# Performance work log

Hardware: AMD Instinct MI355X
Metric: run time of the kernel (lower is better)

The kernel has to match this reference:

```python
import jax, jax.numpy as jnp
import numpy as np

B, S, D, H, E, TOP_K = 4, 2048, 1024, 2048, 8, 2


def setup_inputs() -> dict:
    key = jax.random.key(0)
    ks = jax.random.split(key, 5)
    scale_d = 1.0 / np.sqrt(D)
    scale_h = 1.0 / np.sqrt(H)
    return {
        "x": jax.random.normal(ks[0], (B, S, D), dtype=jnp.float32),
        "gate_w": jax.random.normal(ks[1], (D, E), dtype=jnp.float32) * scale_d,
        "w1": jax.random.normal(ks[2], (E, D, H), dtype=jnp.float32) * scale_d,
        "w2": jax.random.normal(ks[3], (E, D, H), dtype=jnp.float32) * scale_d,
        "w3": jax.random.normal(ks[4], (E, H, D), dtype=jnp.float32) * scale_h,
    }


def reference(x, gate_w, w1, w2, w3):
    # Gating: softmax over experts, keep top-k probs, renormalize.
    gate_scores = jax.nn.softmax(x @ gate_w, axis=-1)          # [B,S,E]
    top_vals, top_idx = jax.lax.top_k(gate_scores, TOP_K)      # [B,S,K]
    mask = (jax.nn.one_hot(top_idx, E, dtype=x.dtype) * top_vals[..., None]).sum(axis=-2)  # [B,S,E]
    weights = mask / (mask.sum(axis=-1, keepdims=True) + 1e-9)
    # Dense SwiGLU over ALL experts (faithful to the original ModuleList loop).
    g = jax.nn.silu(jnp.einsum('bsd,edh->bseh', x, w1)) * jnp.einsum('bsd,edh->bseh', x, w2)  # [B,S,E,H]
    expert_out = jnp.einsum('bseh,ehd->bsed', g, w3)           # [B,S,E,D]
    # Masked weighted combine (dropout is identity in eval / p=0).
    return jnp.einsum('bse,bsed->bsd', weights, expert_out)    # [B,S,D]
```

## Files before the change

### kernel.cpp

```cpp
#include <hip/hip_runtime.h>

#define T_TOK 8192
#define DDIM 1024
#define HDIM 2048
#define NEXP 8

typedef __attribute__((ext_vector_type(8))) short short8;
typedef __attribute__((ext_vector_type(4))) float f32x4;

#define WAITV2 asm volatile("s_waitcnt vmcnt(2)" ::: "memory")
#define WAITV0 asm volatile("s_waitcnt vmcnt(0)" ::: "memory")
#define WAITL0 asm volatile("s_waitcnt lgkmcnt(0)" ::: "memory")
#define SCHEDB __builtin_amdgcn_sched_barrier(0)
#define BARRIER __builtin_amdgcn_s_barrier()

__device__ __forceinline__ unsigned short f2bf(float f) {
  unsigned int u = __builtin_bit_cast(unsigned int, f);
  u += 0x7fffu + ((u >> 16) & 1u);
  return (unsigned short)(u >> 16);
}
__device__ __forceinline__ float bf2f(unsigned short h) {
  unsigned int u = ((unsigned int)h) << 16;
  return __builtin_bit_cast(float, u);
}
__device__ __forceinline__ void gload16(const void* g, void* l) {
  __builtin_amdgcn_global_load_lds((const __attribute__((address_space(1))) void*)g,
                                   (__attribute__((address_space(3))) void*)l, 16, 0, 0);
}
__device__ __forceinline__ int imin(int a, int b) { return a < b ? a : b; }

__global__ __launch_bounds__(256) void cvt_kernel(const float* __restrict__ in,
                                                  unsigned short* __restrict__ out, int n) {
  int i = (blockIdx.x * 256 + threadIdx.x) * 8;
  int stride = gridDim.x * 256 * 8;
  for (; i < n; i += stride) {
    float4 a = *(const float4*)(in + i);
    float4 b = *(const float4*)(in + i + 4);
    alignas(16) unsigned short t[8] = {f2bf(a.x), f2bf(a.y), f2bf(a.z), f2bf(a.w),
                                       f2bf(b.x), f2bf(b.y), f2bf(b.z), f2bf(b.w)};
    *(uint4*)(out + i) = *(const uint4*)t;
  }
}

__global__ __launch_bounds__(256) void tcvt_kernel(const float* __restrict__ in,
                                                   unsigned short* __restrict__ out,
                                                   int R, int C, size_t outEstride,
                                                   int perm, int s16) {
  int e = blockIdx.z;
  int rb = blockIdx.y * 64, cb = blockIdx.x * 64;
  const float* inE = in + (size_t)e * R * C;
  unsigned short* outE = out + (size_t)e * outEstride;
  __shared__ float tile[64][65];
  int tid = threadIdx.x;
  #pragma unroll
  for (int i = 0; i < 4; ++i) {
    int f = tid + i * 256;
    int r = f >> 4, c4 = (f & 15) << 2;
    float4 v = *(const float4*)(inE + (size_t)(rb + r) * C + cb + c4);
    tile[r][c4] = v.x; tile[r][c4 + 1] = v.y; tile[r][c4 + 2] = v.z; tile[r][c4 + 3] = v.w;
  }
  __syncthreads();
  #pragma unroll
  for (int i = 0; i < 2; ++i) {
    int g = tid + i * 256;
    int oc = g >> 3;
    int r8 = (g & 7) << 3;
    alignas(16) unsigned short tmp[8];
    #pragma unroll
    for (int j = 0; j < 8; ++j) tmp[j] = f2bf(tile[r8 + j][oc]);
    int orow = cb + oc;
    int orow2 = perm ? (32 * (orow >> 4) + (orow & 15) + s16) : orow;
    *(uint4*)(outE + (size_t)orow2 * R + rb + r8) = *(const uint4*)tmp;
  }
}

__global__ __launch_bounds__(256) void gate_kernel(const float* __restrict__ x,
                                                   const float* __restrict__ gw,
                                                   int* __restrict__ t_exp,
                                                   float* __restrict__ t_w) {
  int t = blockIdx.x * 4 + (threadIdx.x >> 6);
  int lane = threadIdx.x & 63;
  const float* xp = x + (size_t)t * DDIM;
  float acc[NEXP];
  #pragma unroll
  for (int e = 0; e < NEXP; ++e) acc[e] = 0.f;
  for (int i = 0; i < DDIM / 64; ++i) {
    int d = i * 64 + lane;
    float xv = xp[d];
    const float* g = gw + d * NEXP;
    #pragma unroll
    for (int e = 0; e < NEXP; ++e) acc[e] += xv * g[e];
  }
  #pragma unroll
  for (int off = 32; off > 0; off >>= 1) {
    #pragma unroll
    for (int e = 0; e < NEXP; ++e) acc[e] += __shfl_xor(acc[e], off, 64);
  }
  float mx = acc[0];
  #pragma unroll
  for (int e = 1; e < NEXP; ++e) mx = fmaxf(mx, acc[e]);
  float p[NEXP]; float S = 0.f;
  #pragma unroll
  for (int e = 0; e < NEXP; ++e) { p[e] = expf(acc[e] - mx); S += p[e]; }
  int i0 = 0; float v0 = p[0];
  #pragma unroll
  for (int e = 1; e < NEXP; ++e) if (p[e] > v0) { v0 = p[e]; i0 = e; }
  int i1 = -1; float v1 = -1.f;
  #pragma unroll
  for (int e = 0; e < NEXP; ++e) if (e != i0 && p[e] > v1) { v1 = p[e]; i1 = e; }
  float pv0 = v0 / S, pv1 = v1 / S;
  float denom = pv0 + pv1 + 1e-9f;
  if (lane == 0) {
    t_exp[t * 2] = i0; t_exp[t * 2 + 1] = i1;
    t_w[t * 2] = pv0 / denom; t_w[t * 2 + 1] = pv1 / denom;
  }
}

__global__ __launch_bounds__(1024) void partition_kernel(
    const int* __restrict__ t_exp, const float* __restrict__ t_w,
    int* __restrict__ ctrl, int* __restrict__ row_tok,
    float* __restrict__ row_w, int* __restrict__ inv_row) {
  int tid = threadIdx.x;
  int wv = tid >> 6, lane = tid & 63;
  __shared__ int wtot[16][8];
  __shared__ int wbase[16][8];
  __shared__ int soff[8];

  int t0 = tid * 8;
  int exps[16];
  int c[8];
  #pragma unroll
  for (int e = 0; e < 8; ++e) c[e] = 0;
  #pragma unroll
  for (int s = 0; s < 16; ++s) {
    exps[s] = t_exp[t0 * 2 + s];
    #pragma unroll
    for (int e = 0; e < 8; ++e) c[e] += (exps[s] == e);
  }
  int inc[8];
  #pragma unroll
  for (int e = 0; e < 8; ++e) inc[e] = c[e];
  #pragma unroll
  for (int d = 1; d < 64; d <<= 1) {
    #pragma unroll
    for (int e = 0; e < 8; ++e) {
      int v = __shfl_up(inc[e], d, 64);
      if (lane >= d) inc[e] += v;
    }
  }
  if (lane == 63) {
    #pragma unroll
    for (int e = 0; e < 8; ++e) wtot[wv][e] = inc[e];
  }
  __syncthreads();
  if (wv == 0 && lane < 16) {
    #pragma unroll
    for (int e = 0; e < 8; ++e) {
      int b = 0;
      for (int w = 0; w < 16; ++w)
        if (w < lane) b += wtot[w][e];
      wbase[lane][e] = b;
    }
  }
  __syncthreads();
  if (tid == 0) {
    int o = 0;
    #pragma unroll
    for (int e = 0; e < 8; ++e) {
      int tot = wbase[15][e] + wtot[15][e];
      ctrl[e] = tot; ctrl[8 + e] = o; soff[e] = o; o += tot;
    }
  }
  __syncthreads();
  int base[8];
  #pragma unroll
  for (int e = 0; e < 8; ++e) base[e] = soff[e] + wbase[wv][e] + (inc[e] - c[e]);
  #pragma unroll
  for (int s = 0; s < 16; ++s) {
    int ee = exps[s];
    float w = t_w[t0 * 2 + s];
    int pos = 0;
    #pragma unroll
    for (int e = 0; e < 8; ++e)
      if (ee == e) { pos = base[e]; base[e] = base[e] + 1; }
    row_tok[pos] = t0 + (s >> 1);
    row_w[pos] = w;
    inv_row[t0 * 2 + s] = pos;
  }
}


#define PHASE(B_, KS_, MH_, STG) do {                                      \
    short8 av[4];                                                          \
    if (MH_ == 0) {                                                        \
      _Pragma("unroll")                                                    \
      for (int n = 0; n < 4; ++n)                                          \
        bv[n] = *(const short8*)(&lds[B_][1][0] + bR + cK[KS_] + n * 1024);\
    }                                                                      \
    _Pragma("unroll")                                                      \
    for (int m = 0; m < 4; ++m)                                            \
      av[m] = *(const short8*)(&lds[B_][0][0] + aR + cK[KS_] + (MH_ * 4 + m) * 1024); \
    STG;                                                                   \
    WAITV2;                                                                \
    BARRIER;                                                               \
    WAITL0; SCHEDB;                                                        \
    __builtin_amdgcn_s_setprio(1);                                         \
    _Pragma("unroll")                                                      \
    for (int m = 0; m < 4; ++m)                                            \
      _Pragma("unroll")                                                    \
      for (int n = 0; n < 4; ++n)                                          \
        acc[MH_ * 4 + m][n] = __builtin_amdgcn_mfma_f32_16x16x32_bf16(av[m], bv[n], acc[MH_ * 4 + m][n], 0, 0, 0); \
    __builtin_amdgcn_s_setprio(0);                                         \
    BARRIER;                                                               \
} while (0)

#define K_PIPELINE(NT)                                                     \
  WAITV0;                                                                  \
  STB(0, 0, 0); STB(0, 1, 0); STB(0, 2, 0); STB(0, 3, 0);                  \
  STA(0, 0, 0); STA(0, 1, 0); STA(0, 2, 0); STA(0, 3, 0);                  \
  WAITV0; BARRIER;                                                         \
  _Pragma("unroll 1")                                                      \
  for (int kt = 0; kt < (NT); kt += 2) {                                   \
    int t1 = kt + 1;                                                       \
    int t2 = imin(kt + 2, (NT) - 1);                                       \
    PHASE(0, 0, 0, { STB(1, 0, t1); STB(1, 1, t1); });                     \
    PHASE(0, 0, 1, { STB(1, 2, t1); STB(1, 3, t1); });                     \
    PHASE(0, 1, 0, { STA(1, 0, t1); STA(1, 2, t1); });                     \
    PHASE(0, 1, 1, { STA(1, 1, t1); STA(1, 3, t1); });                     \
    PHASE(1, 0, 0, { STB(0, 0, t2); STB(0, 1, t2); });                     \
    PHASE(1, 0, 1, { STB(0, 2, t2); STB(0, 3, t2); });                     \
    PHASE(1, 1, 0, { STA(0, 0, t2); STA(0, 2, t2); });                     \
    PHASE(1, 1, 1, { STA(0, 1, t2); STA(0, 3, t2); });                     \
  }

__global__ __launch_bounds__(512, 1) void gemm1_kernel(
    const unsigned short* __restrict__ xbf,
    const unsigned short* __restrict__ w12t,
    const int* __restrict__ row_tok, const float* __restrict__ row_w,
    const int* __restrict__ ctrl, unsigned short* __restrict__ G) {
  int bid = blockIdx.x;
  int e = bid & 7;
  int j = bid >> 3;
  int nt = ((j >> 5) << 2) | (j & 3);
  int mt0 = (j >> 2) & 7;
  int cnt = ctrl[e];
  if (mt0 * 256 >= cnt) return;
  int off = ctrl[8 + e];

  __shared__ unsigned short lds[2][2][16384];

  int tid = threadIdx.x, lane = tid & 63;
  const unsigned short* w12e = w12t + (size_t)e * (4096 * 1024);

  int sr = tid >> 3;
  int cS8 = ((tid & 7) ^ (sr & 7)) * 8;
  const unsigned short* bQ = w12e + (size_t)(nt * 256 + sr) * 1024 + cS8;

  int wid = tid >> 6, wr = wid >> 2, wc = wid & 3;
  int lr16 = lane & 15, hi = lane >> 4;
  int cK[2] = { ((hi) ^ (lr16 & 7)) * 8, ((4 | hi) ^ (lr16 & 7)) * 8 };
  int aR = (wr * 128 + lr16) * 64;
  int bR = (wc * 64 + lr16) * 64;

#define STA(B_, Q_, KT) gload16(aQ[Q_] + (KT) * 64, &lds[B_][0][0] + (Q_) * 4096 + tid * 8)
#define STB(B_, Q_, KT) gload16(bQ + (Q_) * 65536 + (KT) * 64, &lds[B_][1][0] + (Q_) * 4096 + tid * 8)

  #pragma unroll 1
  for (int mt = mt0; mt * 256 < cnt; mt += 8) {
    const unsigned short* aQ[4];
    #pragma unroll
    for (int q = 0; q < 4; ++q) {
      int tok = row_tok[off + imin(mt * 256 + q * 64 + sr, cnt - 1)];
      aQ[q] = xbf + (size_t)tok * 1024 + cS8;
    }
    f32x4 z = {0.f, 0.f, 0.f, 0.f};
    f32x4 acc[8][4];
    #pragma unroll
    for (int m = 0; m < 8; ++m)
      #pragma unroll
      for (int n = 0; n < 4; ++n) acc[m][n] = z;
    short8 bv[4];

    K_PIPELINE(16)

    #pragma unroll
    for (int m = 0; m < 8; ++m)
      #pragma unroll
      for (int jj = 0; jj < 4; ++jj) {
        int rl = mt * 256 + ((m >> 2) ? (64 + wr * 128) : (wr * 128)) + (m & 3) * 16 + hi * 4 + jj;
        rl = mt * 256 + wr * 128 + (m >> 2) * 64 + (m & 3) * 16 + hi * 4 + jj;
        if (rl < cnt) {
          float wrj = row_w[off + rl];
          size_t base = (size_t)(off + rl) * HDIM + nt * 128 + wc * 32 + lr16;
          float h1 = acc[m][0][jj], h2 = acc[m][1][jj];
          G[base] = f2bf((h1 / (1.f + __expf(-h1))) * h2 * wrj);
          h1 = acc[m][2][jj]; h2 = acc[m][3][jj];
          G[base + 16] = f2bf((h1 / (1.f + __expf(-h1))) * h2 * wrj);
        }
      }
  }
#undef STA
#undef STB
}

__global__ __launch_bounds__(512, 1) void gemm2_kernel(
    const unsigned short* __restrict__ G,
    const unsigned short* __restrict__ w3t,
    const int* __restrict__ ctrl, unsigned short* __restrict__ Y) {
  int bid = blockIdx.x;
  int e = bid & 7;
  int j = bid >> 3;
  int nt = j >> 3;
  int mt0 = j & 7;
  int cnt = ctrl[e];
  if (mt0 * 256 >= cnt) return;
  int off = ctrl[8 + e];

  __shared__ unsigned short lds[2][2][16384];

  int tid = threadIdx.x, lane = tid & 63;
  const unsigned short* w3e = w3t + (size_t)e * (1024 * 2048);

  int sr = tid >> 3;
  int cS8 = ((tid & 7) ^ (sr & 7)) * 8;
  const unsigned short* bQ = w3e + (size_t)(nt * 256 + sr) * 2048 + cS8;

  int wid = tid >> 6, wr = wid >> 2, wc = wid & 3;
  int lr16 = lane & 15, hi = lane >> 4;
  int cK[2] = { ((hi) ^ (lr16 & 7)) * 8, ((4 | hi) ^ (lr16 & 7)) * 8 };
  int aR = (wr * 128 + lr16) * 64;
  int bR = (wc * 64 + lr16) * 64;

#define STA(B_, Q_, KT) gload16(aQ[Q_] + (KT) * 64, &lds[B_][0][0] + (Q_) * 4096 + tid * 8)
#define STB(B_, Q_, KT) gload16(bQ + (Q_) * 131072 + (KT) * 64, &lds[B_][1][0] + (Q_) * 4096 + tid * 8)

  #pragma unroll 1
  for (int mt = mt0; mt * 256 < cnt; mt += 8) {
    const unsigned short* aQ[4];
    #pragma unroll
    for (int q = 0; q < 4; ++q)
      aQ[q] = G + (size_t)(off + imin(mt * 256 + q * 64 + sr, cnt - 1)) * 2048 + cS8;

    f32x4 z = {0.f, 0.f, 0.f, 0.f};
    f32x4 acc[8][4];
    #pragma unroll
    for (int m = 0; m < 8; ++m)
      #pragma unroll
      for (int n = 0; n < 4; ++n) acc[m][n] = z;
    short8 bv[4];

    K_PIPELINE(32)

    #pragma unroll
    for (int m = 0; m < 8; ++m)
      #pragma unroll
      for (int jj = 0; jj < 4; ++jj) {
        int rl = mt * 256 + wr * 128 + (m >> 2) * 64 + (m & 3) * 16 + hi * 4 + jj;
        if (rl < cnt) {
          size_t yrow = (size_t)(off + rl) * DDIM + nt * 256 + wc * 64 + lr16;
          #pragma unroll
          for (int n = 0; n < 4; ++n) Y[yrow + n * 16] = f2bf(acc[m][n][jj]);
        }
      }
  }
#undef STA
#undef STB
}

__global__ __launch_bounds__(256) void combine_kernel(const unsigned short* __restrict__ Y,
                                                      const int* __restrict__ inv_row,
                                                      float* __restrict__ out) {
  int gid = blockIdx.x * 256 + threadIdx.x;
  int t = gid >> 7;
  int cidx = (gid & 127) * 8;
  int rA = inv_row[t * 2], rB = inv_row[t * 2 + 1];
  uint4 va = *(const uint4*)(Y + (size_t)rA * DDIM + cidx);
  uint4 vb = *(const uint4*)(Y + (size_t)rB * DDIM + cidx);
  const unsigned short* pa = (const unsigned short*)&va;
  const unsigned short* pb = (const unsigned short*)&vb;
  float4 o0, o1;
  o0.x = bf2f(pa[0]) + bf2f(pb[0]); o0.y = bf2f(pa[1]) + bf2f(pb[1]);
  o0.z = bf2f(pa[2]) + bf2f(pb[2]); o0.w = bf2f(pa[3]) + bf2f(pb[3]);
  o1.x = bf2f(pa[4]) + bf2f(pb[4]); o1.y = bf2f(pa[5]) + bf2f(pb[5]);
  o1.z = bf2f(pa[6]) + bf2f(pb[6]); o1.w = bf2f(pa[7]) + bf2f(pb[7]);
  float* op = out + (size_t)t * DDIM + cidx;
  *(float4*)op = o0;
  *(float4*)(op + 4) = o1;
}

extern "C" void kernel_launch(void* const* d_in, const int* in_sizes, int n_in,
                              void* d_out, int out_size, void* d_ws, size_t ws_size,
                              hipStream_t stream) {
  const float* x  = (const float*)d_in[0];
  const float* gw = (const float*)d_in[1];
  const float* w1 = (const float*)d_in[2];
  const float* w2 = (const float*)d_in[3];
  const float* w3 = (const float*)d_in[4];
  float* out = (float*)d_out;
  char* ws = (char*)d_ws;

  unsigned short* xbf  = (unsigned short*)(ws + 0);
  unsigned short* w12t = (unsigned short*)(ws + 16777216);
  unsigned short* w3t  = (unsigned short*)(ws + 83886080);
  unsigned short* G    = (unsigned short*)(ws + 117440512);
  unsigned short* Y    = (unsigned short*)(ws + 184549376);
  int*   row_tok = (int*)  (ws + 218103808);
  float* row_w   = (float*)(ws + 218169344);
  int*   inv_row = (int*)  (ws + 218234880);
  int*   t_exp   = (int*)  (ws + 218300416);
  float* t_w     = (float*)(ws + 218365952);
  int*   ctrl    = (int*)  (ws + 218431488);

  cvt_kernel<<<4096, 256, 0, stream>>>(x, xbf, T_TOK * DDIM);
  tcvt_kernel<<<dim3(32, 16, 8), 256, 0, stream>>>(w1, w12t, 1024, 2048,
                                                   (size_t)4096 * 1024, 1, 0);
  tcvt_kernel<<<dim3(32, 16, 8), 256, 0, stream>>>(w2, w12t, 1024, 2048,
                                                   (size_t)4096 * 1024, 1, 16);
  tcvt_kernel<<<dim3(16, 32, 8), 256, 0, stream>>>(w3, w3t, 2048, 1024,
                                                   (size_t)1024 * 2048, 0, 0);

  gate_kernel<<<2048, 256, 0, stream>>>(x, gw, t_exp, t_w);
  partition_kernel<<<1, 1024, 0, stream>>>(t_exp, t_w, ctrl, row_tok, row_w, inv_row);

  gemm1_kernel<<<1024, 512, 0, stream>>>(xbf, w12t, row_tok, row_w, ctrl, G);
  gemm2_kernel<<<256, 512, 0, stream>>>(G, w3t, ctrl, Y);
  combine_kernel<<<4096, 256, 0, stream>>>(Y, inv_row, out);
}
```

Measured before the change: 390.6 us.

## Switch GEMM k-loop to 4-stage LDS pipeline with 32-wide K tiles

Replaces the double-buffered 64-wide K tiles with a four-buffer ring of 32-wide K tiles, prefetching three tiles ahead and waiting with vmcnt(8) instead of vmcnt(2). The LDS swizzle and load addressing are redone for the narrower 32-element rows, and the loop now runs twice as many iterations per tile. The goal is to keep more global loads in flight so memory latency is hidden behind MFMA work. In exchange there are twice as many barriers per unit of K and each phase does less MFMA work.

```diff
diff --git a/kernel.cpp b/kernel.cpp
--- a/kernel.cpp
+++ b/kernel.cpp
@@ -8,7 +8,7 @@
 typedef __attribute__((ext_vector_type(8))) short short8;
 typedef __attribute__((ext_vector_type(4))) float f32x4;
 
-#define WAITV2 asm volatile("s_waitcnt vmcnt(2)" ::: "memory")
+#define WAITV8 asm volatile("s_waitcnt vmcnt(8)" ::: "memory")
 #define WAITV0 asm volatile("s_waitcnt vmcnt(0)" ::: "memory")
 #define WAITL0 asm volatile("s_waitcnt lgkmcnt(0)" ::: "memory")
 #define SCHEDB __builtin_amdgcn_sched_barrier(0)
@@ -190,18 +190,18 @@
 }
 
 
-#define PHASE(B_, KS_, MH_, STG) do {                                      \
+#define PHASE(BUF, MH_, STG) do {                                          \
     short8 av[4];                                                          \
     if (MH_ == 0) {                                                        \
       _Pragma("unroll")                                                    \
       for (int n = 0; n < 4; ++n)                                          \
-        bv[n] = *(const short8*)(&lds[B_][1][0] + bR + cK[KS_] + n * 1024);\
+        bv[n] = *(const short8*)(&lds[BUF][1][0] + bOff + n * 512);        \
     }                                                                      \
     _Pragma("unroll")                                                      \
     for (int m = 0; m < 4; ++m)                                            \
-      av[m] = *(const short8*)(&lds[B_][0][0] + aR + cK[KS_] + (MH_ * 4 + m) * 1024); \
+      av[m] = *(const short8*)(&lds[BUF][0][0] + aOff + (MH_ * 4 + m) * 512); \
     STG;                                                                   \
-    WAITV2;                                                                \
+    WAITV8;                                                                \
     BARRIER;                                                               \
     WAITL0; SCHEDB;                                                        \
     __builtin_amdgcn_s_setprio(1);                                         \
@@ -214,23 +214,27 @@
     BARRIER;                                                               \
 } while (0)
 
+#define STA(SB, KO) do {                                                   \
+    gload16(aQ0 + (KO), &lds[SB][0][0] + tid * 8);                         \
+    gload16(aQ1 + (KO), &lds[SB][0][0] + 4096 + tid * 8); } while (0)
+#define STB(SB, KO) do {                                                   \
+    gload16(bQ0 + (KO), &lds[SB][1][0] + tid * 8);                         \
+    gload16(bQ1 + (KO), &lds[SB][1][0] + 4096 + tid * 8); } while (0)
+
 #define K_PIPELINE(NT)                                                     \
   WAITV0;                                                                  \
-  STB(0, 0, 0); STB(0, 1, 0); STB(0, 2, 0); STB(0, 3, 0);                  \
-  STA(0, 0, 0); STA(0, 1, 0); STA(0, 2, 0); STA(0, 3, 0);                  \
-  WAITV0; BARRIER;                                                         \
+  STA(0, 0);  STB(0, 0);                                                   \
+  STA(1, 32); STB(1, 32);                                                  \
+  STA(2, 64); STB(2, 64);                                                  \
+  WAITV8; BARRIER;                                                         \
   _Pragma("unroll 1")                                                      \
-  for (int kt = 0; kt < (NT); kt += 2) {                                   \
-    int t1 = kt + 1;                                                       \
-    int t2 = imin(kt + 2, (NT) - 1);                                       \
-    PHASE(0, 0, 0, { STB(1, 0, t1); STB(1, 1, t1); });                     \
-    PHASE(0, 0, 1, { STB(1, 2, t1); STB(1, 3, t1); });                     \
-    PHASE(0, 1, 0, { STA(1, 0, t1); STA(1, 2, t1); });                     \
-    PHASE(0, 1, 1, { STA(1, 1, t1); STA(1, 3, t1); });                     \
-    PHASE(1, 0, 0, { STB(0, 0, t2); STB(0, 1, t2); });                     \
-    PHASE(1, 0, 1, { STB(0, 2, t2); STB(0, 3, t2); });                     \
-    PHASE(1, 1, 0, { STA(0, 0, t2); STA(0, 2, t2); });                     \
-    PHASE(1, 1, 1, { STA(0, 1, t2); STA(0, 3, t2); });                     \
+  for (int t = 0; t < (NT); ++t) {                                         \
+    int buf = t & 3;                                                       \
+    int tc = imin(t + 3, (NT) - 1);                                        \
+    int sb = tc & 3;                                                       \
+    int ko = tc * 32;                                                      \
+    PHASE(buf, 0, STA(sb, ko));                                            \
+    PHASE(buf, 1, STB(sb, ko));                                            \
   }
 
 __global__ __launch_bounds__(512, 1) void gemm1_kernel(
@@ -247,32 +251,29 @@
   if (mt0 * 256 >= cnt) return;
   int off = ctrl[8 + e];
 
-  __shared__ unsigned short lds[2][2][16384];
+  __shared__ unsigned short lds[4][2][8192];
 
   int tid = threadIdx.x, lane = tid & 63;
   const unsigned short* w12e = w12t + (size_t)e * (4096 * 1024);
 
-  int sr = tid >> 3;
-  int cS8 = ((tid & 7) ^ (sr & 7)) * 8;
-  const unsigned short* bQ = w12e + (size_t)(nt * 256 + sr) * 1024 + cS8;
+  int sr = tid >> 2;
+  int cS8 = ((tid & 3) ^ (sr & 3) ^ ((sr >> 2) & 3)) * 8;
+  const unsigned short* bQ0 = w12e + (size_t)(nt * 256 + sr) * 1024 + cS8;
+  const unsigned short* bQ1 = w12e + (size_t)(nt * 256 + 128 + sr) * 1024 + cS8;
 
   int wid = tid >> 6, wr = wid >> 2, wc = wid & 3;
   int lr16 = lane & 15, hi = lane >> 4;
-  int cK[2] = { ((hi) ^ (lr16 & 7)) * 8, ((4 | hi) ^ (lr16 & 7)) * 8 };
-  int aR = (wr * 128 + lr16) * 64;
-  int bR = (wc * 64 + lr16) * 64;
-
-#define STA(B_, Q_, KT) gload16(aQ[Q_] + (KT) * 64, &lds[B_][0][0] + (Q_) * 4096 + tid * 8)
-#define STB(B_, Q_, KT) gload16(bQ + (Q_) * 65536 + (KT) * 64, &lds[B_][1][0] + (Q_) * 4096 + tid * 8)
+  int klane = (lr16 & 3) ^ ((lr16 >> 2) & 3);
+  int aOff = (wr * 128 + lr16) * 32 + ((hi ^ klane) * 8);
+  int bOff = (wc * 64 + lr16) * 32 + ((hi ^ klane) * 8);
 
   #pragma unroll 1
   for (int mt = mt0; mt * 256 < cnt; mt += 8) {
-    const unsigned short* aQ[4];
-    #pragma unroll
-    for (int q = 0; q < 4; ++q) {
-      int tok = row_tok[off + imin(mt * 256 + q * 64 + sr, cnt - 1)];
-      aQ[q] = xbf + (size_t)tok * 1024 + cS8;
-    }
+    int tokA = row_tok[off + imin(mt * 256 + sr, cnt - 1)];
+    int tokB = row_tok[off + imin(mt * 256 + 128 + sr, cnt - 1)];
+    const unsigned short* aQ0 = xbf + (size_t)tokA * 1024 + cS8;
+    const unsigned short* aQ1 = xbf + (size_t)tokB * 1024 + cS8;
+
     f32x4 z = {0.f, 0.f, 0.f, 0.f};
     f32x4 acc[8][4];
     #pragma unroll
@@ -281,14 +282,13 @@
       for (int n = 0; n < 4; ++n) acc[m][n] = z;
     short8 bv[4];
 
-    K_PIPELINE(16)
+    K_PIPELINE(32)
 
     #pragma unroll
     for (int m = 0; m < 8; ++m)
       #pragma unroll
       for (int jj = 0; jj < 4; ++jj) {
-        int rl = mt * 256 + ((m >> 2) ? (64 + wr * 128) : (wr * 128)) + (m & 3) * 16 + hi * 4 + jj;
-        rl = mt * 256 + wr * 128 + (m >> 2) * 64 + (m & 3) * 16 + hi * 4 + jj;
+        int rl = mt * 256 + wr * 128 + (m >> 2) * 64 + (m & 3) * 16 + hi * 4 + jj;
         if (rl < cnt) {
           float wrj = row_w[off + rl];
           size_t base = (size_t)(off + rl) * HDIM + nt * 128 + wc * 32 + lr16;
@@ -299,8 +299,6 @@
         }
       }
   }
-#undef STA
-#undef STB
 }
 
 __global__ __launch_bounds__(512, 1) void gemm2_kernel(
@@ -316,30 +314,28 @@
   if (mt0 * 256 >= cnt) return;
   int off = ctrl[8 + e];
 
-  __shared__ unsigned short lds[2][2][16384];
+  __shared__ unsigned short lds[4][2][8192];
 
   int tid = threadIdx.x, lane = tid & 63;
   const unsigned short* w3e = w3t + (size_t)e * (1024 * 2048);
 
-  int sr = tid >> 3;
-  int cS8 = ((tid & 7) ^ (sr & 7)) * 8;
-  const unsigned short* bQ = w3e + (size_t)(nt * 256 + sr) * 2048 + cS8;
+  int sr = tid >> 2;
+  int cS8 = ((tid & 3) ^ (sr & 3) ^ ((sr >> 2) & 3)) * 8;
+  const unsigned short* bQ0 = w3e + (size_t)(nt * 256 + sr) * 2048 + cS8;
+  const unsigned short* bQ1 = w3e + (size_t)(nt * 256 + 128 + sr) * 2048 + cS8;
 
   int wid = tid >> 6, wr = wid >> 2, wc = wid & 3;
   int lr16 = lane & 15, hi = lane >> 4;
-  int cK[2] = { ((hi) ^ (lr16 & 7)) * 8, ((4 | hi) ^ (lr16 & 7)) * 8 };
-  int aR = (wr * 128 + lr16) * 64;
-  int bR = (wc * 64 + lr16) * 64;
-
-#define STA(B_, Q_, KT) gload16(aQ[Q_] + (KT) * 64, &lds[B_][0][0] + (Q_) * 4096 + tid * 8)
-#define STB(B_, Q_, KT) gload16(bQ + (Q_) * 131072 + (KT) * 64, &lds[B_][1][0] + (Q_) * 4096 + tid * 8)
+  int klane = (lr16 & 3) ^ ((lr16 >> 2) & 3);
+  int aOff = (wr * 128 + lr16) * 32 + ((hi ^ klane) * 8);
+  int bOff = (wc * 64 + lr16) * 32 + ((hi ^ klane) * 8);
 
   #pragma unroll 1
   for (int mt = mt0; mt * 256 < cnt; mt += 8) {
-    const unsigned short* aQ[4];
-    #pragma unroll
-    for (int q = 0; q < 4; ++q)
-      aQ[q] = G + (size_t)(off + imin(mt * 256 + q * 64 + sr, cnt - 1)) * 2048 + cS8;
+    const unsigned short* aQ0 =
+        G + (size_t)(off + imin(mt * 256 + sr, cnt - 1)) * 2048 + cS8;
+    const unsigned short* aQ1 =
+        G + (size_t)(off + imin(mt * 256 + 128 + sr, cnt - 1)) * 2048 + cS8;
 
     f32x4 z = {0.f, 0.f, 0.f, 0.f};
     f32x4 acc[8][4];
@@ -349,7 +345,7 @@
       for (int n = 0; n < 4; ++n) acc[m][n] = z;
     short8 bv[4];
 
-    K_PIPELINE(32)
+    K_PIPELINE(64)
 
     #pragma unroll
     for (int m = 0; m < 8; ++m)
@@ -363,8 +359,6 @@
         }
       }
   }
-#undef STA
-#undef STB
 }
 
 __global__ __launch_bounds__(256) void combine_kernel(const unsigned short* __restrict__ Y,
```

After: 421.6 us. 7.9% more time.
